# Optimization experiments

Hardware: AMD Instinct MI355X
Metric: run time of the kernel (lower is better)

The kernel has to match this reference:

```python
import jax, jax.numpy as jnp
import numpy as np

N, T, D, H = 128, 64, 1024, 1024
DA = 4  # hard-coded 4x4 attention grid


def setup_inputs() -> dict:
    key = jax.random.key(0)
    ks = jax.random.split(key, 6)
    x = jax.random.normal(ks[0], (N, T, D), dtype=jnp.float32)
    A = jax.random.normal(ks[1], (N, H, DA, DA), dtype=jnp.float32)
    Wx = jax.random.normal(ks[2], (D, 4 * H), dtype=jnp.float32) / np.sqrt(D)
    Wh = jax.random.normal(ks[3], (H, 4 * H), dtype=jnp.float32) / np.sqrt(H)
    Wattn = jax.random.normal(ks[4], (H, 4 * H), dtype=jnp.float32) / np.sqrt(H)
    b = jnp.zeros((4 * H,), dtype=jnp.float32)
    return {"x": x, "A": A, "Wx": Wx, "Wh": Wh, "Wattn": Wattn, "b": b}


def reference(x, A, Wx, Wh, Wattn, b):
    n, h_dim, da, _ = A.shape
    Af = A.reshape(n, h_dim, da * da)          # (N, H, P) with P = 16
    h0 = A.mean(axis=(2, 3))                   # global image feature init
    c0 = h0
    scale = jnp.sqrt(jnp.asarray(h_dim, x.dtype))

    def step(carry, xt):
        h, c = carry
        # scaled dot-product attention over P=16 spatial positions
        scores = jnp.einsum('nh,nhp->np', h, Af) / scale   # (N, P)
        w = jax.nn.softmax(scores, axis=1)
        attn = jnp.einsum('nhp,np->nh', Af, w)             # (N, H)
        # fused LSTM gates
        act = xt @ Wx + h @ Wh + attn @ Wattn + b          # (N, 4H)
        i, f, o, g = jnp.split(act, 4, axis=1)
        i = jax.nn.sigmoid(i)
        f = jax.nn.sigmoid(f)
        o = jax.nn.sigmoid(o)
        g = jnp.tanh(g)
        c_next = f * c + i * g
        h_next = o * jnp.tanh(c_next)
        return (h_next, c_next), h_next

    _, hs = jax.lax.scan(step, (h0, c0), jnp.swapaxes(x, 0, 1))  # (T, N, H)
    return jnp.swapaxes(hs, 0, 1)                                # (N, T, H)
```

## Files before the change

### kernel.cpp

```cpp
#include <hip/hip_runtime.h>
#include <hip/hip_bf16.h>
#include <cmath>

#define N_   128
#define T_   64
#define D_   1024
#define H_   1024
#define G4_  4096

typedef short bf16x8  __attribute__((ext_vector_type(8)));
typedef float f32x4   __attribute__((ext_vector_type(4)));
typedef float f32x16  __attribute__((ext_vector_type(16)));

__device__ __forceinline__ unsigned short f2bf(float f) {
    union { float f; unsigned int u; } v; v.f = f;
    unsigned int r = (v.u + 0x7FFFu + ((v.u >> 16) & 1u)) >> 16;
    return (unsigned short)r;
}
__device__ __forceinline__ float bf2f(unsigned short s) {
    union { unsigned int u; float f; } v; v.u = ((unsigned int)s) << 16;
    return v.f;
}



__global__ void k_pack_w(const float* __restrict__ src, unsigned short* __restrict__ dst,
                         int kcoff, int kctot) {
    __shared__ float ld[64][33];
    int j0 = blockIdx.x * 32, k0 = blockIdx.y * 64;
    int tid = threadIdx.x;
    int c = tid & 31, r = tid >> 5;
    #pragma unroll
    for (int i = 0; i < 8; i++)
        ld[r + i * 8][c] = src[(long)(k0 + r + i * 8) * G4_ + j0 + c];
    __syncthreads();
    int j = tid & 31, ku = tid >> 5;
    int kcl = ku >> 2, kg = ku & 3;
    int jti = (j0 + j) >> 4, cl = (j0 + j) & 15;
    int kc = kcoff + (k0 >> 5) + kcl;
    unsigned short q[8];
    #pragma unroll
    for (int e = 0; e < 8; e++) q[e] = f2bf(ld[ku * 8 + e][j]);
    *(uint4*)(dst + ((long)(jti * kctot + kc) * 64 + kg * 16 + cl) * 8) = *(uint4*)q;
}

__global__ void k_pack_w32(const float* __restrict__ src, unsigned short* __restrict__ dst) {
    __shared__ float ld[64][33];
    int j0 = blockIdx.x * 32, k0 = blockIdx.y * 64;
    int tid = threadIdx.x;
    int c = tid & 31, r = tid >> 5;
    #pragma unroll
    for (int i = 0; i < 8; i++)
        ld[r + i * 8][c] = src[(long)(k0 + r + i * 8) * G4_ + j0 + c];
    __syncthreads();
    int cl = tid & 31, kgrp = (tid >> 5) & 1, kcl = tid >> 6;
    int kc = (k0 >> 4) + kcl;
    unsigned short q[8];
    #pragma unroll
    for (int e = 0; e < 8; e++) q[e] = f2bf(ld[kcl * 16 + kgrp * 8 + e][cl]);
    *(uint4*)(dst + (((long)blockIdx.x * 64 + kc) * 64 + kgrp * 32 + cl) * 8) = *(uint4*)q;
}

__global__ void k_pack_x32(const float* __restrict__ x, unsigned short* __restrict__ xP32) {
    long gid = (long)blockIdx.x * 256 + threadIdx.x;
    int mm = (int)(gid >> 7), u = (int)(gid & 127);
    const float* src = x + (long)mm * 1024 + u * 8;
    int n = mm >> 6, t = mm & 63;
    int tile = t * 4 + (n >> 5);
    int row = n & 31;
    int kc = u >> 1, kgrp = u & 1;
    float4 a = *(const float4*)src, b = *(const float4*)(src + 4);
    unsigned short q[8] = {f2bf(a.x), f2bf(a.y), f2bf(a.z), f2bf(a.w),
                           f2bf(b.x), f2bf(b.y), f2bf(b.z), f2bf(b.w)};
    *(uint4*)(xP32 + (((long)tile * 64 + kc) * 64 + kgrp * 32 + row) * 8) = *(uint4*)q;
}

__global__ void k_pack_af32(const float* __restrict__ A, unsigned short* __restrict__ AfP32,
                            unsigned short* __restrict__ Af2) {
    __shared__ float ld[64][17];
    int n = blockIdx.x, h0 = blockIdx.y * 64;
    int tid = threadIdx.x;
    int hh = tid >> 2, pq = tid & 3;
    float4 v = *(const float4*)(A + ((long)n * H_ + h0 + hh) * 16 + pq * 4);
    unsigned short o[4] = {f2bf(v.x), f2bf(v.y), f2bf(v.z), f2bf(v.w)};
    *(uint2*)(Af2 + ((long)n * H_ + h0 + hh) * 16 + pq * 4) = *(uint2*)o;
    ld[hh][pq * 4 + 0] = v.x; ld[hh][pq * 4 + 1] = v.y;
    ld[hh][pq * 4 + 2] = v.z; ld[hh][pq * 4 + 3] = v.w;
    __syncthreads();
    if (tid < 128) {
        int p = tid >> 3, ku = tid & 7;
        int kc = (h0 >> 4) + (ku >> 1), kgrp = ku & 1;
        int row = (n & 1) * 16 + p;
        unsigned short q[8];
        #pragma unroll
        for (int e = 0; e < 8; e++) q[e] = f2bf(ld[ku * 8 + e][p]);
        *(uint4*)(AfP32 + (((long)(n >> 1) * 64 + kc) * 64 + kgrp * 32 + row) * 8) = *(uint4*)q;
    }
}

__global__ void k_h0(const float* __restrict__ A, float* __restrict__ h,
                     float* __restrict__ c, unsigned short* __restrict__ hP0) {
    long id = (long)blockIdx.x * 256 + threadIdx.x;
    const float4* ap = (const float4*)(A + id * 16);
    float s = 0.f;
    #pragma unroll
    for (int q = 0; q < 4; q++) { float4 v = ap[q]; s += v.x + v.y + v.z + v.w; }
    float m = s * (1.0f / 16.0f);
    h[id] = m; c[id] = m;
    int n = (int)(id >> 10), j = (int)(id & 1023);
    hP0[((long)((n >> 4) * 32 + (j >> 5)) * 64 + ((j >> 3) & 3) * 16 + (n & 15)) * 8 + (j & 7)] = f2bf(m);
}

__global__ __launch_bounds__(512)
void k_part0(const float* __restrict__ hbuf, const unsigned short* __restrict__ Af2,
             float* __restrict__ partial0) {
    int n = blockIdx.x;
    int tid = threadIdx.x;
    int jh = tid * 2;
    float sp[16];
    #pragma unroll
    for (int p = 0; p < 16; p++) sp[p] = 0.f;
    #pragma unroll
    for (int u = 0; u < 2; u++) {
        float hv = hbuf[(long)n * H_ + jh + u];
        const unsigned short* afp = Af2 + ((long)n * H_ + jh + u) * 16;
        bf16x8 a0 = *(const bf16x8*)(afp);
        bf16x8 a1 = *(const bf16x8*)(afp + 8);
        #pragma unroll
        for (int p = 0; p < 8; p++) { sp[p] += hv * bf2f((unsigned short)a0[p]);
                                      sp[8+p] += hv * bf2f((unsigned short)a1[p]); }
    }
    #pragma unroll
    for (int off = 1; off < 8; off <<= 1) {
        #pragma unroll
        for (int p = 0; p < 16; p++) sp[p] += __shfl_xor(sp[p], off);
    }
    int jt = tid >> 3;
    if ((tid & 7) == 0) {
        #pragma unroll
        for (int p = 0; p < 16; p++)
            partial0[((long)n * 16 + p) * 64 + jt] = sp[p];
    }
}

__global__ __launch_bounds__(64)
void k_score_tiny(const float* __restrict__ partial, float* __restrict__ wbuf) {
    int n = blockIdx.x;
    int lane = threadIdx.x;
    int p = lane & 15, c4 = lane >> 4;
    const float* src = partial + ((long)n * 16 + p) * 64 + c4 * 16;
    float s = 0.f;
    #pragma unroll
    for (int q = 0; q < 16; q++) s += src[q];
    s += __shfl_xor(s, 16);
    s += __shfl_xor(s, 32);
    s *= (1.0f / 32.0f);
    float m = s;
    #pragma unroll
    for (int off = 1; off < 16; off <<= 1) m = fmaxf(m, __shfl_xor(m, off));
    float e = expf(s - m);
    float sum = e;
    #pragma unroll
    for (int off = 1; off < 16; off <<= 1) sum += __shfl_xor(sum, off);
    if (c4 == 0) wbuf[n * 16 + p] = e / sum;
}

__global__ __launch_bounds__(256, 2)
void k_aw(const unsigned short* __restrict__ AfP32, const unsigned short* __restrict__ WattnP32,
          unsigned short* __restrict__ AW) {
    int tid = threadIdx.x;
    int wv = tid >> 6, lane = tid & 63;
    int wr = wv >> 1, wc = wv & 1;
    int at0 = blockIdx.x * 4 + wr * 2;
    int jt0 = blockIdx.y * 4 + wc * 2;

    f32x16 acc[2][2];
    #pragma unroll
    for (int i = 0; i < 2; i++)
        #pragma unroll
        for (int j = 0; j < 2; j++)
            #pragma unroll
            for (int r = 0; r < 16; r++) acc[i][j][r] = 0.f;

    const unsigned short* apx[2];
    const unsigned short* bpx[2];
    #pragma unroll
    for (int i = 0; i < 2; i++) {
        apx[i] = AfP32     + (long)(at0 + i) * (64 * 512) + lane * 8;
        bpx[i] = WattnP32  + (long)(jt0 + i) * (64 * 512) + lane * 8;
    }
    #pragma unroll 2
    for (int kc = 0; kc < 64; kc++) {
        bf16x8 a[2], b[2];
        #pragma unroll
        for (int i = 0; i < 2; i++) a[i] = *(const bf16x8*)(apx[i] + kc * 512);
        #pragma unroll
        for (int i = 0; i < 2; i++) b[i] = *(const bf16x8*)(bpx[i] + kc * 512);
        #pragma unroll
        for (int i = 0; i < 2; i++)
            #pragma unroll
            for (int j = 0; j < 2; j++)
                acc[i][j] = __builtin_amdgcn_mfma_f32_32x32x16_bf16(a[i], b[j], acc[i][j], 0, 0, 0);
    }
    int col_l = lane & 31, rbase = 4 * (lane >> 5);
    #pragma unroll
    for (int i = 0; i < 2; i++) {
        #pragma unroll
        for (int j = 0; j < 2; j++) {
            int col = (jt0 + j) * 32 + col_l;
            #pragma unroll
            for (int r = 0; r < 16; r++) {
                int grow = (at0 + i) * 32 + (r & 3) + 8 * (r >> 2) + rbase;
                int n = grow >> 4, p = grow & 15;
                AW[((long)n * G4_ + col) * 16 + p] = f2bf(acc[i][j][r]);
            }
        }
    }
}

__global__ __launch_bounds__(256, 2)
void k_actx(const unsigned short* __restrict__ xP32, const unsigned short* __restrict__ WxP32,
            unsigned short* __restrict__ actx) {
    int tid = threadIdx.x;
    int wv = tid >> 6, lane = tid & 63;
    int wr = wv >> 1, wc = wv & 1;
    int at0 = blockIdx.x * 4 + wr * 2;
    int jt0 = blockIdx.y * 4 + wc * 2;

    f32x16 acc[2][2];
    #pragma unroll
    for (int i = 0; i < 2; i++)
        #pragma unroll
        for (int j = 0; j < 2; j++)
            #pragma unroll
            for (int r = 0; r < 16; r++) acc[i][j][r] = 0.f;

    const unsigned short* apx[2];
    const unsigned short* bpx[2];
    #pragma unroll
    for (int i = 0; i < 2; i++) {
        apx[i] = xP32  + (long)(at0 + i) * (64 * 512) + lane * 8;
        bpx[i] = WxP32 + (long)(jt0 + i) * (64 * 512) + lane * 8;
    }
    #pragma unroll 2
    for (int kc = 0; kc < 64; kc++) {
        bf16x8 a[2], b[2];
        #pragma unroll
        for (int i = 0; i < 2; i++) a[i] = *(const bf16x8*)(apx[i] + kc * 512);
        #pragma unroll
        for (int i = 0; i < 2; i++) b[i] = *(const bf16x8*)(bpx[i] + kc * 512);
        #pragma unroll
        for (int i = 0; i < 2; i++)
            #pragma unroll
            for (int j = 0; j < 2; j++)
                acc[i][j] = __builtin_amdgcn_mfma_f32_32x32x16_bf16(a[i], b[j], acc[i][j], 0, 0, 0);
    }
    int col_l = lane & 31, rbase = 4 * (lane >> 5);
    #pragma unroll
    for (int i = 0; i < 2; i++) {
        #pragma unroll
        for (int j = 0; j < 2; j++) {
            int col = (jt0 + j) * 32 + col_l;
            #pragma unroll
            for (int r = 0; r < 16; r++) {
                long m = (long)(at0 + i) * 32 + (r & 3) + 8 * (r >> 2) + rbase;
                actx[m * G4_ + col] = f2bf(acc[i][j][r]);
            }
        }
    }
}


__global__ __launch_bounds__(512, 2)
void k_step(const unsigned short* __restrict__ actx,
            const unsigned short* __restrict__ hPin,
            unsigned short* __restrict__ hPout,
            const unsigned short* __restrict__ WhP,
            const unsigned short* __restrict__ AW,
            const unsigned short* __restrict__ Af2,
            const float* __restrict__ wbuf,
            const float* __restrict__ bvec,
            float* __restrict__ c,
            float* __restrict__ partOUT,
            float* __restrict__ out, int t) {
    int tid = threadIdx.x;
    int wv = tid >> 6, lane = tid & 63;
    int ks = wv & 3, rh = wv >> 2;
    int cl = lane & 15, kg = lane >> 4;
    int jt = blockIdx.x;
    int nt2 = blockIdx.y;
    int colbase = jt * 16;

    f32x4 acc[4];
    #pragma unroll
    for (int g = 0; g < 4; g++) acc[g] = (f32x4){0.f, 0.f, 0.f, 0.f};

    const unsigned short* abase = hPin + ((long)(nt2 * 2 + rh) * 32 + ks * 8) * 512 + lane * 8;
    const unsigned short* bb[4];
    #pragma unroll
    for (int g = 0; g < 4; g++)
        bb[g] = WhP + ((long)(g * 64 + jt) * 32 + ks * 8) * 512 + lane * 8;

    #pragma unroll
    for (int i = 0; i < 8; i++) {
        bf16x8 a = *(const bf16x8*)(abase + i * 512);
        #pragma unroll
        for (int g = 0; g < 4; g++) {
            bf16x8 b = *(const bf16x8*)(bb[g] + i * 512);
            acc[g] = __builtin_amdgcn_mfma_f32_16x16x32_bf16(a, b, acc[g], 0, 0, 0);
        }
    }

    __shared__ float red[3][2][64][17];
    __shared__ float act[4][32][17];
    if (ks != 0) {
        #pragma unroll
        for (int g = 0; g < 4; g++)
            #pragma unroll
            for (int v = 0; v < 4; v++) red[ks - 1][rh][lane][g * 4 + v] = acc[g][v];
    }
    __syncthreads();
    if (ks == 0) {
        #pragma unroll
        for (int g = 0; g < 4; g++)
            #pragma unroll
            for (int v = 0; v < 4; v++) {
                float s = acc[g][v] + red[0][rh][lane][g*4+v] + red[1][rh][lane][g*4+v]
                        + red[2][rh][lane][g*4+v];
                act[g][rh * 16 + kg * 4 + v][cl] = s;
            }
    }
    __syncthreads();

    int nloc = tid >> 4, jl = tid & 15;
    int n = nt2 * 32 + nloc, jh = colbase + jl;
    float wv16[16];
    #pragma unroll
    for (int p = 0; p < 16; p++) wv16[p] = wbuf[n * 16 + p];

    long rm = (long)(t * 8 + (n >> 4)) * 16 + (n & 15);
    float s4[4];
    #pragma unroll
    for (int g = 0; g < 4; g++) {
        int j = g * 1024 + jh;
        const unsigned short* awp = AW + ((long)n * G4_ + j) * 16;
        bf16x8 aw0 = *(const bf16x8*)(awp);
        bf16x8 aw1 = *(const bf16x8*)(awp + 8);
        float at = 0.f;
        #pragma unroll
        for (int p = 0; p < 8; p++) at += wv16[p]     * bf2f((unsigned short)aw0[p]);
        #pragma unroll
        for (int p = 0; p < 8; p++) at += wv16[8 + p] * bf2f((unsigned short)aw1[p]);
        s4[g] = act[g][nloc][jl] + bf2f(actx[rm * G4_ + j]) + at + bvec[j];
    }
    float ig = 1.f / (1.f + expf(-s4[0]));
    float fg = 1.f / (1.f + expf(-s4[1]));
    float og = 1.f / (1.f + expf(-s4[2]));
    float gg = tanhf(s4[3]);
    long idx = (long)n * H_ + jh;
    float cn = fg * c[idx] + ig * gg;
    float hn = og * tanhf(cn);
    c[idx] = cn;
    out[((long)n * T_ + t) * H_ + jh] = hn;
    hPout[((long)((n >> 4) * 32 + (jh >> 5)) * 64 + ((jh >> 3) & 3) * 16 + (n & 15)) * 8 + (jh & 7)] = f2bf(hn);

    const unsigned short* afp = Af2 + ((long)n * H_ + jh) * 16;
    bf16x8 af0 = *(const bf16x8*)(afp);
    bf16x8 af1 = *(const bf16x8*)(afp + 8);
    float sp[16];
    #pragma unroll
    for (int p = 0; p < 8; p++) { sp[p]     = hn * bf2f((unsigned short)af0[p]);
                                  sp[8 + p] = hn * bf2f((unsigned short)af1[p]); }
    #pragma unroll
    for (int off = 1; off < 16; off <<= 1) {
        #pragma unroll
        for (int p = 0; p < 16; p++) sp[p] += __shfl_xor(sp[p], off);
    }
    float outv = 0.f;
    #pragma unroll
    for (int p = 0; p < 16; p++) if (jl == p) outv = sp[p];
    partOUT[((long)n * 16 + jl) * 64 + jt] = outv;
}


extern "C" void kernel_launch(void* const* d_in, const int* in_sizes, int n_in,
                              void* d_out, int out_size, void* d_ws, size_t ws_size,
                              hipStream_t stream) {
    const float* x     = (const float*)d_in[0];
    const float* A     = (const float*)d_in[1];
    const float* Wx    = (const float*)d_in[2];
    const float* Wh    = (const float*)d_in[3];
    const float* Wattn = (const float*)d_in[4];
    const float* b     = (const float*)d_in[5];
    float* out = (float*)d_out;

    char* ws = (char*)d_ws;
    size_t off = 0;
    auto alloc = [&](size_t bytes) -> void* {
        void* p = ws + off;
        off += (bytes + 255) & ~(size_t)255;
        return p;
    };
    unsigned short* xP32   = (unsigned short*)alloc((size_t)256 * 64 * 512 * 2);
    unsigned short* WxP32  = (unsigned short*)alloc((size_t)128 * 64 * 512 * 2);
    unsigned short* WhP    = (unsigned short*)alloc((size_t)256 * 32 * 512 * 2);
    unsigned short* WatP32 = (unsigned short*)alloc((size_t)128 * 64 * 512 * 2);
    unsigned short* AfP32  = (unsigned short*)alloc((size_t)64 * 64 * 512 * 2);
    unsigned short* Af2    = (unsigned short*)alloc((size_t)N_ * H_ * 16 * 2);
    unsigned short* AW     = (unsigned short*)alloc((size_t)N_ * G4_ * 16 * 2);
    unsigned short* actx   = (unsigned short*)alloc((size_t)8192 * G4_ * 2);
    float*          hbuf   = (float*)alloc((size_t)N_ * H_ * 4);
    float*          cbuf   = (float*)alloc((size_t)N_ * H_ * 4);
    unsigned short* hP0    = (unsigned short*)alloc((size_t)8 * 32 * 512 * 2);
    unsigned short* hP1    = (unsigned short*)alloc((size_t)8 * 32 * 512 * 2);
    float*          part0  = (float*)alloc((size_t)N_ * 16 * 64 * 4);
    float*          part1  = (float*)alloc((size_t)N_ * 16 * 64 * 4);
    float*          wbuf   = (float*)alloc((size_t)N_ * 16 * 4);

    k_pack_w32<<<dim3(128, 16), dim3(256), 0, stream>>>(Wx,    WxP32);
    k_pack_w  <<<dim3(128, 16), dim3(256), 0, stream>>>(Wh,    WhP, 0, 32);
    k_pack_w32<<<dim3(128, 16), dim3(256), 0, stream>>>(Wattn, WatP32);
    k_pack_x32<<<dim3(4096), dim3(256), 0, stream>>>(x, xP32);
    k_pack_af32<<<dim3(128, 16), dim3(256), 0, stream>>>(A, AfP32, Af2);
    k_h0<<<dim3(512), dim3(256), 0, stream>>>(A, hbuf, cbuf, hP0);
    k_part0<<<dim3(N_), dim3(512), 0, stream>>>(hbuf, Af2, part0);
    k_aw<<<dim3(16, 32), dim3(256), 0, stream>>>(AfP32, WatP32, AW);
    k_actx<<<dim3(64, 32), dim3(256), 0, stream>>>(xP32, WxP32, actx);

    for (int t = 0; t < T_; t++) {
        unsigned short* hin  = (t & 1) ? hP1 : hP0;
        unsigned short* hout = (t & 1) ? hP0 : hP1;
        float* pIN  = (t & 1) ? part1 : part0;
        float* pOUT = (t & 1) ? part0 : part1;
        k_score_tiny<<<dim3(N_), dim3(64), 0, stream>>>(pIN, wbuf);
        k_step<<<dim3(64, 4), dim3(512), 0, stream>>>(actx, hin, hout, WhP, AW, Af2,
                                                      wbuf, b, cbuf, pOUT, out, t);
    }
}
```

Measured before the change: 1.035 ms.

## Fuse attention softmax into step kernel and accumulate scores with atomics

Removes the per-timestep k_score_tiny launch. Each k_step block now computes the softmax over the 16 attention scores in shared memory. The score partials are accumulated straight into a small buffer with atomicAdd instead of being written per column tile and reduced in a separate pass. A three-buffer rotation keeps one buffer for reading, one for accumulating and one being zeroed, which avoids a separate reset step. The cost is 64 atomics landing on each score address per step, redundant softmax work in every block, and non-deterministic float summation order.

```diff
diff --git a/kernel.cpp b/kernel.cpp
--- a/kernel.cpp
+++ b/kernel.cpp
@@ -144,7 +144,7 @@
 }
 
 __global__ __launch_bounds__(64)
-void k_score_tiny(const float* __restrict__ partial, float* __restrict__ wbuf) {
+void k_red0(const float* __restrict__ partial, float* __restrict__ p0) {
     int n = blockIdx.x;
     int lane = threadIdx.x;
     int p = lane & 15, c4 = lane >> 4;
@@ -154,15 +154,11 @@
     for (int q = 0; q < 16; q++) s += src[q];
     s += __shfl_xor(s, 16);
     s += __shfl_xor(s, 32);
-    s *= (1.0f / 32.0f);
-    float m = s;
-    #pragma unroll
-    for (int off = 1; off < 16; off <<= 1) m = fmaxf(m, __shfl_xor(m, off));
-    float e = expf(s - m);
-    float sum = e;
-    #pragma unroll
-    for (int off = 1; off < 16; off <<= 1) sum += __shfl_xor(sum, off);
-    if (c4 == 0) wbuf[n * 16 + p] = e / sum;
+    if (c4 == 0) p0[n * 16 + p] = s;
+}
+
+__global__ void k_zerobuf(float* __restrict__ p) {
+    p[blockIdx.x * 1024 + threadIdx.x] = 0.f;
 }
 
 __global__ __launch_bounds__(256, 2)
@@ -278,10 +274,11 @@
             const unsigned short* __restrict__ WhP,
             const unsigned short* __restrict__ AW,
             const unsigned short* __restrict__ Af2,
-            const float* __restrict__ wbuf,
+            const float* __restrict__ pRead,
+            float* __restrict__ pAcc,
+            float* __restrict__ pZero,
             const float* __restrict__ bvec,
             float* __restrict__ c,
-            float* __restrict__ partOUT,
             float* __restrict__ out, int t) {
     int tid = threadIdx.x;
     int wv = tid >> 6, lane = tid & 63;
@@ -291,6 +288,25 @@
     int nt2 = blockIdx.y;
     int colbase = jt * 16;
 
+    __shared__ float red[3][2][64][17];
+    __shared__ float act[4][32][17];
+    __shared__ float wsm[32][17];
+
+    {
+        int nloc_f = tid >> 4, jl_f = tid & 15;
+        int n_f = nt2 * 32 + nloc_f;
+        float s = pRead[n_f * 16 + jl_f] * (1.0f / 32.0f);
+        float m = s;
+        #pragma unroll
+        for (int off = 1; off < 16; off <<= 1) m = fmaxf(m, __shfl_xor(m, off));
+        float e = expf(s - m);
+        float sum = e;
+        #pragma unroll
+        for (int off = 1; off < 16; off <<= 1) sum += __shfl_xor(sum, off);
+        wsm[nloc_f][jl_f] = e / sum;
+        if (jt == 0) pZero[nt2 * 512 + tid] = 0.f;
+    }
+
     f32x4 acc[4];
     #pragma unroll
     for (int g = 0; g < 4; g++) acc[g] = (f32x4){0.f, 0.f, 0.f, 0.f};
@@ -311,8 +327,6 @@
         }
     }
 
-    __shared__ float red[3][2][64][17];
-    __shared__ float act[4][32][17];
     if (ks != 0) {
         #pragma unroll
         for (int g = 0; g < 4; g++)
@@ -336,7 +350,7 @@
     int n = nt2 * 32 + nloc, jh = colbase + jl;
     float wv16[16];
     #pragma unroll
-    for (int p = 0; p < 16; p++) wv16[p] = wbuf[n * 16 + p];
+    for (int p = 0; p < 16; p++) wv16[p] = wsm[nloc][p];
 
     long rm = (long)(t * 8 + (n >> 4)) * 16 + (n & 15);
     float s4[4];
@@ -379,7 +393,7 @@
     float outv = 0.f;
     #pragma unroll
     for (int p = 0; p < 16; p++) if (jl == p) outv = sp[p];
-    partOUT[((long)n * 16 + jl) * 64 + jt] = outv;
+    atomicAdd(&pAcc[n * 16 + jl], outv);
 }
 
 
@@ -413,9 +427,8 @@
     float*          cbuf   = (float*)alloc((size_t)N_ * H_ * 4);
     unsigned short* hP0    = (unsigned short*)alloc((size_t)8 * 32 * 512 * 2);
     unsigned short* hP1    = (unsigned short*)alloc((size_t)8 * 32 * 512 * 2);
-    float*          part0  = (float*)alloc((size_t)N_ * 16 * 64 * 4);
-    float*          part1  = (float*)alloc((size_t)N_ * 16 * 64 * 4);
-    float*          wbuf   = (float*)alloc((size_t)N_ * 16 * 4);
+    float*          scr    = (float*)alloc((size_t)N_ * 16 * 64 * 4);
+    float*          pb     = (float*)alloc((size_t)3 * N_ * 16 * 4);
 
     k_pack_w32<<<dim3(128, 16), dim3(256), 0, stream>>>(Wx,    WxP32);
     k_pack_w  <<<dim3(128, 16), dim3(256), 0, stream>>>(Wh,    WhP, 0, 32);
@@ -423,17 +436,19 @@
     k_pack_x32<<<dim3(4096), dim3(256), 0, stream>>>(x, xP32);
     k_pack_af32<<<dim3(128, 16), dim3(256), 0, stream>>>(A, AfP32, Af2);
     k_h0<<<dim3(512), dim3(256), 0, stream>>>(A, hbuf, cbuf, hP0);
-    k_part0<<<dim3(N_), dim3(512), 0, stream>>>(hbuf, Af2, part0);
+    k_part0<<<dim3(N_), dim3(512), 0, stream>>>(hbuf, Af2, scr);
+    k_red0<<<dim3(N_), dim3(64), 0, stream>>>(scr, pb);
+    k_zerobuf<<<dim3(4), dim3(1024), 0, stream>>>(pb + 2048);
     k_aw<<<dim3(16, 32), dim3(256), 0, stream>>>(AfP32, WatP32, AW);
     k_actx<<<dim3(64, 32), dim3(256), 0, stream>>>(xP32, WxP32, actx);
 
     for (int t = 0; t < T_; t++) {
         unsigned short* hin  = (t & 1) ? hP1 : hP0;
         unsigned short* hout = (t & 1) ? hP0 : hP1;
-        float* pIN  = (t & 1) ? part1 : part0;
-        float* pOUT = (t & 1) ? part0 : part1;
-        k_score_tiny<<<dim3(N_), dim3(64), 0, stream>>>(pIN, wbuf);
+        float* pRead = pb + (t % 3) * 2048;
+        float* pAcc  = pb + ((t + 1) % 3) * 2048;
+        float* pZero = pb + ((t + 2) % 3) * 2048;
         k_step<<<dim3(64, 4), dim3(512), 0, stream>>>(actx, hin, hout, WhP, AW, Af2,
-                                                      wbuf, b, cbuf, pOUT, out, t);
-    }
-}
+                                                      pRead, pAcc, pZero, b, cbuf, out, t);
+    }
+}
```

New measurement: 907.3 us. 12.3% less time.
